# Kernel optimization log

Hardware: AMD Instinct MI355X
Metric: run time of the kernel (lower is better)

The kernel has to match this reference:

```python
import jax, jax.numpy as jnp
import numpy as np

L = 3264          # seq_length
K = 12            # ktc=4 -> K=12
LOCC = 4          # ktc=4 -> Locc=4
BLK = 12          # mmse_block_size
DMIN, DMAX = -10, 10  # delay_search_range
RHO = 0.9         # assumed frequency-correlation coefficient for MMSE C matrix


def setup_inputs() -> dict:
    key = jax.random.key(0)
    k1, k2, k3 = jax.random.split(key, 3)
    ls_real = jax.random.normal(k1, (L,), dtype=jnp.float32)
    ls_imag = jax.random.normal(k2, (L,), dtype=jnp.float32)
    cyclic_shifts = jax.random.randint(k3, (8, 4), 0, K, dtype=jnp.int32)
    return {"ls_real": ls_real, "ls_imag": ls_imag, "cyclic_shifts": cyclic_shifts}


def _estimate(ls, cs_flat):
    P = cs_flat.shape[0]  # total ports across all users
    ideal = ((K - cs_flat) % K) * (L // K)                      # [P] ideal CIR peak positions
    h_time = jnp.fft.ifft(ls)
    hmag = jnp.abs(h_time)                                      # [L]
    idx = jnp.arange(L)
    # circular search window [ideal+DMIN, ideal+DMAX] around each ideal peak
    rel = (idx[None, :] - (ideal[:, None] + DMIN)) % L          # [P, L]
    mask = rel <= (DMAX - DMIN)
    vals = jnp.where(mask, hmag[None, :], -jnp.inf)
    peak = jnp.argmax(vals, axis=1)                             # [P]
    d = peak - ideal
    offset = jnp.where((peak > ideal) & (d > L // 2), d - L,
             jnp.where((ideal - peak) > L // 2, d + L, d))
    m = offset + ideal                                          # [P] phasor shift amounts
    # phasor exp(j 2 pi m n / L); reduce m*n mod L to keep fp32 phase accurate
    n = jnp.arange(L)
    phase = (2.0 * np.pi / L) * ((m[:, None] * n[None, :]) % L).astype(jnp.float32)
    phasor = jnp.exp(1j * phase).astype(jnp.complex64)          # [P, L]
    h_up = ls[None, :] * phasor                                 # [P, L]
    # OCC demux: average every LOCC points
    h_avg = h_up.reshape(P, L // LOCC, LOCC).mean(axis=-1)      # [P, L/LOCC]
    # linear interpolation back to L, centers of groups as sample points
    g = LOCC
    orig = (g - 1) / 2.0 + g * jnp.arange(L // g, dtype=jnp.float32)
    new = jnp.arange(L, dtype=jnp.float32)
    interp1 = jax.vmap(lambda r: jnp.interp(new, orig, r))
    h_interp = (interp1(jnp.real(h_avg)) + 1j * interp1(jnp.imag(h_avg))).astype(jnp.complex64)  # [P, L]
    # residual of multi-port reconstruction
    h_recon = jnp.sum(h_interp / phasor, axis=0)
    residual = ls - h_recon
    # noise power from adjacent-tone differences
    diff = ls[1:] - ls[:-1]
    noise_power = jnp.mean(jnp.abs(diff) ** 2) / 2.0
    # add residual back per port
    h_wr = h_interp + residual[None, :] * phasor                # [P, L]
    # block MMSE: h_mmse = C (C + noise I)^{-1} h_block, C[i,j] = rho^{|i-j|}
    ij = jnp.abs(jnp.arange(BLK)[:, None] - jnp.arange(BLK)[None, :])
    C = (RHO ** ij).astype(jnp.float32)
    A = C + noise_power * jnp.eye(BLK, dtype=jnp.float32)
    F = jnp.linalg.solve(A.T, C.T).T                            # F = C @ inv(A), [BLK, BLK]
    blocks = h_wr.reshape(P, L // BLK, BLK)
    h_mmse = jnp.einsum('pbk,jk->pbj', blocks, F.astype(jnp.complex64)).reshape(P, L)
    # the original nested loop emits the same P inner results for each of P outer (u,p)
    return jnp.tile(h_mmse, (P, 1))                             # [P*P, L]


def reference(ls_real, ls_imag, cyclic_shifts):
    ls = (ls_real + 1j * ls_imag).astype(jnp.complex64)
    cs_flat = cyclic_shifts.reshape(-1)
    return _estimate(ls, cs_flat)
```

## Files before the change

kernel.cpp:

```cpp
#include <hip/hip_runtime.h>
#include <math.h>

#define LL    3264
#define KK    12
#define PP    32
#define NW    21
#define DMIN  (-10)
#define GAVG  (LL/4)
#define NBLK  (LL/12)

#define OUT_REAL  (PP*PP*LL)
#define OUT_CPLX  (PP*PP*LL*2)
#define SCRATCH_F 270520

__global__ void k_window_noise(const float* __restrict__ lsr,
                               const float* __restrict__ lsi,
                               const int* __restrict__ cs,
                               double* __restrict__ mag2,
                               double* __restrict__ noise) {
    __shared__ double sre[256], sim[256];
    const int b = blockIdx.x;
    const int tid = threadIdx.x;
    const float c0 = (float)(2.0 * M_PI / (double)LL);
    if (b < PP * NW) {
        const int p = b / NW, r = b % NW;
        const int ideal = ((KK - cs[p]) % KK) * (LL / KK);
        int t = ideal + DMIN + r;
        t %= LL; if (t < 0) t += LL;
        double are = 0.0, aim = 0.0;
        for (int n = tid; n < LL; n += 256) {
            unsigned mod = (unsigned)(n * t) % LL;
            float ang = c0 * (float)mod;
            float ss, cc;
            sincosf(ang, &ss, &cc);
            float xr = lsr[n], xi = lsi[n];
            are += (double)(xr * cc - xi * ss);
            aim += (double)(xr * ss + xi * cc);
        }
        sre[tid] = are; sim[tid] = aim;
        __syncthreads();
        for (int s = 128; s > 0; s >>= 1) {
            if (tid < s) { sre[tid] += sre[tid + s]; sim[tid] += sim[tid + s]; }
            __syncthreads();
        }
        if (tid == 0) mag2[b] = sre[0] * sre[0] + sim[0] * sim[0];
    } else {
        double acc = 0.0;
        for (int n = tid; n < LL - 1; n += 256) {
            double dr = (double)lsr[n + 1] - (double)lsr[n];
            double di = (double)lsi[n + 1] - (double)lsi[n];
            acc += dr * dr + di * di;
        }
        sre[tid] = acc;
        __syncthreads();
        for (int s = 128; s > 0; s >>= 1) {
            if (tid < s) sre[tid] += sre[tid + s];
            __syncthreads();
        }
        if (tid == 0) *noise = sre[0] / (double)(LL - 1) * 0.5;
    }
}

__global__ void k_peak_F(const int* __restrict__ cs,
                         const double* __restrict__ mag2,
                         const double* __restrict__ noise,
                         int* __restrict__ peak,
                         float* __restrict__ F) {
    __shared__ double A[12][12], Y[12][12];
    const int tid = threadIdx.x;

    if (tid < PP) {
        const int ideal = ((KK - cs[tid]) % KK) * (LL / KK);
        double best = -1.0; int bestl = 0x7fffffff;
        for (int r = 0; r < NW; r++) {
            int l = ideal + DMIN + r;
            l %= LL; if (l < 0) l += LL;
            double v = mag2[tid * NW + r];
            if (v > best || (v == best && l < bestl)) { best = v; bestl = l; }
        }
        peak[tid] = bestl;
    }

    const int row = tid / 12, c = tid % 12;
    if (tid < 144) {
        int d = row - c; if (d < 0) d = -d;
        float cij = (float)pow(0.9, (double)d);
        double npow = (double)((float)(*noise));
        A[row][c] = (double)cij + (row == c ? npow : 0.0);
        Y[row][c] = (double)cij;
    }
    __syncthreads();

    for (int col = 0; col < 12; col++) {
        double dinv = 0.0, pa = 0.0, py = 0.0, f = 0.0;
        if (tid < 144) {
            dinv = 1.0 / A[col][col];
            pa = A[col][c]; py = Y[col][c];
            f  = A[row][col];
        }
        __syncthreads();
        if (tid < 144) {
            if (row == col) { A[row][c] = pa * dinv; Y[row][c] = py * dinv; }
            else            { A[row][c] -= (f * dinv) * pa; Y[row][c] -= (f * dinv) * py; }
        }
        __syncthreads();
    }
    if (tid < 144) F[row * 12 + c] = (float)Y[c][row];
}

template <bool CPLX>
__global__ __launch_bounds__(384) void k_fused(const float* __restrict__ lsr,
                                               const float* __restrict__ lsi,
                                               const int* __restrict__ peak,
                                               const float* __restrict__ F,
                                               float* __restrict__ out) {
    const int b = blockIdx.x;
    const int tid = threadIdx.x;
    __shared__ float hav[32][5][2];
    __shared__ float hin[32][12][2];
    __shared__ float pha[32][12][2];
    __shared__ float con[32][12][2];
    __shared__ float w_s[32][12][2];
    __shared__ float res[12][2];
    __shared__ float Fs[144];
    __shared__ int   pk[32];

    if (tid < 144) Fs[tid] = F[tid];
    if (tid < 32)  pk[tid] = peak[tid];
    __syncthreads();

    const int jb3 = 3 * b - 1;
    const int jbase = jb3 < 0 ? 0 : jb3;
    const float c0 = (float)(2.0 * M_PI / (double)LL);

    if (tid < 160) {
        const int p = tid / 5, js = tid % 5;
        int j = jbase + js; if (j > GAVG - 1) j = GAVG - 1;
        const int m = pk[p];
        float ar = 0.f, ai = 0.f;
        for (int s = 0; s < 4; s++) {
            int n = j * 4 + s;
            unsigned mod = (unsigned)(m * n) % LL;
            float ang = c0 * (float)mod;
            float ss, cc;
            sincosf(ang, &ss, &cc);
            float xr = lsr[n], xi = lsi[n];
            ar += xr * cc - xi * ss;
            ai += xr * ss + xi * cc;
        }
        hav[p][js][0] = ar * 0.25f;
        hav[p][js][1] = ai * 0.25f;
    }
    __syncthreads();

    {
        const int p = tid / 12, k = tid % 12;
        const int x = b * 12 + k;
        float re, im;
        if (x < 2)            { re = hav[p][0][0]; im = hav[p][0][1]; }
        else if (x >= LL - 2) { int js = (GAVG - 1) - jbase;
                                re = hav[p][js][0]; im = hav[p][js][1]; }
        else {
            int j = (x - 2) >> 2, js = j - jbase;
            float t = ((float)x - (1.5f + 4.0f * (float)j)) * 0.25f;
            float r0 = hav[p][js][0],     i0 = hav[p][js][1];
            float r1 = hav[p][js + 1][0], i1 = hav[p][js + 1][1];
            re = r0 + t * (r1 - r0);
            im = i0 + t * (i1 - i0);
        }
        hin[p][k][0] = re; hin[p][k][1] = im;
        const int m = pk[p];
        unsigned mod = (unsigned)(m * x) % LL;
        float ang = c0 * (float)mod;
        float ss, cc;
        sincosf(ang, &ss, &cc);
        pha[p][k][0] = cc; pha[p][k][1] = ss;
        float den = cc * cc + ss * ss;
        con[p][k][0] = (re * cc + im * ss) / den;
        con[p][k][1] = (im * cc - re * ss) / den;
    }
    __syncthreads();

    if (tid < 24) {
        const int k = tid >> 1, c = tid & 1;
        float s = 0.f;
        for (int p = 0; p < 32; p++) s += con[p][k][c];
        const int n = b * 12 + k;
        res[k][c] = (c ? lsi[n] : lsr[n]) - s;
    }
    __syncthreads();

    {
        const int p = tid / 12, k = tid % 12;
        float rr = res[k][0], ri = res[k][1];
        float cc = pha[p][k][0], ss = pha[p][k][1];
        w_s[p][k][0] = hin[p][k][0] + rr * cc - ri * ss;
        w_s[p][k][1] = hin[p][k][1] + rr * ss + ri * cc;
    }
    __syncthreads();

    {
        const int p = tid / 12, j = tid % 12;
        float ar = 0.f, ai = 0.f;
        for (int k = 0; k < 12; k++) {
            float f = Fs[j * 12 + k];
            ar += f * w_s[p][k][0];
            ai += f * w_s[p][k][1];
        }
        if (CPLX) {
            const size_t off = ((size_t)p * LL + (size_t)b * 12 + j) * 2;
            for (int q = 0; q < PP; q++) {
                out[(size_t)q * PP * LL * 2 + off]     = ar;
                out[(size_t)q * PP * LL * 2 + off + 1] = ai;
            }
        } else {
            const size_t off = (size_t)p * LL + (size_t)b * 12 + j;
            for (int q = 0; q < PP; q++)
                out[(size_t)q * PP * LL + off] = ar;
        }
    }
}

__global__ void k_havg(const float* __restrict__ lsr, const float* __restrict__ lsi,
                       const int* __restrict__ peak, float* __restrict__ havg) {
    const int idx = blockIdx.x * blockDim.x + threadIdx.x;
    if (idx >= PP * GAVG) return;
    const int p = idx / GAVG, jj = idx % GAVG;
    const int m = peak[p];
    const float c0 = (float)(2.0 * M_PI / (double)LL);
    float ar = 0.f, ai = 0.f;
    for (int s = 0; s < 4; s++) {
        int n = jj * 4 + s;
        unsigned mod = (unsigned)(m * n) % LL;
        float ph = c0 * (float)mod;
        float ss, cc;
        sincosf(ph, &ss, &cc);
        float xr = lsr[n], xi = lsi[n];
        ar += xr * cc - xi * ss;
        ai += xr * ss + xi * cc;
    }
    havg[idx * 2]     = ar * 0.25f;
    havg[idx * 2 + 1] = ai * 0.25f;
}

__global__ void k_interp(const float* __restrict__ havg, float* __restrict__ hinterp) {
    const int idx = blockIdx.x * blockDim.x + threadIdx.x;
    if (idx >= PP * LL) return;
    const int p = idx / LL, x = idx % LL;
    const float* hp = havg + (size_t)p * GAVG * 2;
    float re, im;
    if (x < 2) { re = hp[0]; im = hp[1]; }
    else if (x >= LL - 2) { re = hp[(GAVG - 1) * 2]; im = hp[(GAVG - 1) * 2 + 1]; }
    else {
        int j = (x - 2) >> 2;
        float t = ((float)x - (1.5f + 4.0f * (float)j)) * 0.25f;
        float r0 = hp[j * 2],       i0 = hp[j * 2 + 1];
        float r1 = hp[(j + 1) * 2], i1 = hp[(j + 1) * 2 + 1];
        re = r0 + t * (r1 - r0);
        im = i0 + t * (i1 - i0);
    }
    hinterp[idx * 2]     = re;
    hinterp[idx * 2 + 1] = im;
}

__global__ void k_resid(const float* __restrict__ lsr, const float* __restrict__ lsi,
                        const int* __restrict__ peak, const float* __restrict__ hinterp,
                        float* __restrict__ resid) {
    const int l = blockIdx.x * blockDim.x + threadIdx.x;
    if (l >= LL) return;
    const float c0 = (float)(2.0 * M_PI / (double)LL);
    float sr = 0.f, si = 0.f;
    for (int p = 0; p < PP; p++) {
        int m = peak[p];
        unsigned mod = (unsigned)(m * l) % LL;
        float ph = c0 * (float)mod;
        float ss, cc;
        sincosf(ph, &ss, &cc);
        float hr = hinterp[((size_t)p * LL + l) * 2];
        float hi = hinterp[((size_t)p * LL + l) * 2 + 1];
        float den = cc * cc + ss * ss;
        sr += (hr * cc + hi * ss) / den;
        si += (hi * cc - hr * ss) / den;
    }
    resid[l * 2]     = lsr[l] - sr;
    resid[l * 2 + 1] = lsi[l] - si;
}

template <bool CPLX>
__global__ void k_mmse(const int* __restrict__ peak, const float* __restrict__ hinterp,
                       const float* __restrict__ resid, const float* __restrict__ F,
                       float* __restrict__ out) {
    const int idx = blockIdx.x * blockDim.x + threadIdx.x;
    if (idx >= PP * NBLK) return;
    const int p = idx / NBLK, b = idx % NBLK;
    const int m = peak[p];
    const float c0 = (float)(2.0 * M_PI / (double)LL);
    float wr[12], wi[12];
    for (int k = 0; k < 12; k++) {
        int n = b * 12 + k;
        unsigned mod = (unsigned)(m * n) % LL;
        float ph = c0 * (float)mod;
        float ss, cc;
        sincosf(ph, &ss, &cc);
        float rr = resid[n * 2], ri = resid[n * 2 + 1];
        wr[k] = hinterp[((size_t)p * LL + n) * 2]     + (rr * cc - ri * ss);
        wi[k] = hinterp[((size_t)p * LL + n) * 2 + 1] + (rr * ss + ri * cc);
    }
    for (int j = 0; j < 12; j++) {
        float ar = 0.f, ai = 0.f;
        for (int k = 0; k < 12; k++) {
            float f = F[j * 12 + k];
            ar += f * wr[k];
            ai += f * wi[k];
        }
        if (CPLX) {
            float* orow = out + (size_t)p * LL * 2 + (size_t)b * 24;
            orow[j * 2]     = ar;
            orow[j * 2 + 1] = ai;
        } else {
            out[(size_t)p * LL + (size_t)b * 12 + j] = ar;
        }
    }
}

__global__ void k_tile(float4* __restrict__ out, int tile_f4) {
    const int idx = blockIdx.x * blockDim.x + threadIdx.x;
    if (idx >= tile_f4) return;
    float4 v = out[idx];
    for (int q = 1; q < PP; q++)
        out[(size_t)q * tile_f4 + idx] = v;
}

extern "C" void kernel_launch(void* const* d_in, const int* in_sizes, int n_in,
                              void* d_out, int out_size, void* d_ws, size_t ws_size,
                              hipStream_t stream) {
    const float* lsr = (const float*)d_in[0];
    const float* lsi = (const float*)d_in[1];
    const int*   cs  = (const int*)d_in[2];
    float* out = (float*)d_out;
    const bool cplx = (out_size >= OUT_CPLX);

    if (ws_size >= 16384) {
        double* mag2  = (double*)d_ws;
        double* noise = mag2 + PP * NW;
        int*    peak  = (int*)(noise + 1);
        float*  F     = (float*)(peak + PP);

        k_window_noise<<<PP * NW + 1, 256, 0, stream>>>(lsr, lsi, cs, mag2, noise);
        k_peak_F<<<1, 192, 0, stream>>>(cs, mag2, noise, peak, F);
        if (cplx) k_fused<true ><<<NBLK, 384, 0, stream>>>(lsr, lsi, peak, F, out);
        else      k_fused<false><<<NBLK, 384, 0, stream>>>(lsr, lsi, peak, F, out);
    } else {
        float* base = out + ((size_t)out_size - SCRATCH_F);
        double* mag2  = (double*)base;
        double* noise = mag2 + PP * NW;
        int*    peak  = (int*)(base + 2692);
        float*  F     = base + 2724;
        float*  havg  = base + 2868;
        float*  hint  = base + 55092;
        float*  resid = base + 263988;

        k_window_noise<<<PP * NW + 1, 256, 0, stream>>>(lsr, lsi, cs, mag2, noise);
        k_peak_F<<<1, 192, 0, stream>>>(cs, mag2, noise, peak, F);
        k_havg<<<(PP * GAVG + 255) / 256, 256, 0, stream>>>(lsr, lsi, peak, havg);
        k_interp<<<(PP * LL + 255) / 256, 256, 0, stream>>>(havg, hint);
        k_resid<<<(LL + 255) / 256, 256, 0, stream>>>(lsr, lsi, peak, hint, resid);
        if (cplx) {
            k_mmse<true><<<(PP * NBLK + 255) / 256, 256, 0, stream>>>(peak, hint, resid, F, out);
            const int tile_f4 = PP * LL * 2 / 4;
            k_tile<<<(tile_f4 + 255) / 256, 256, 0, stream>>>((float4*)out, tile_f4);
        } else {
            k_mmse<false><<<(PP * NBLK + 255) / 256, 256, 0, stream>>>(peak, hint, resid, F, out);
            const int tile_f4 = PP * LL / 4;
            k_tile<<<(tile_f4 + 255) / 256, 256, 0, stream>>>((float4*)out, tile_f4);
        }
    }
}
```

Before: 28.23 us.

## Dedupe window DFTs by ideal, fuse peak/F solve, vectorize tiled output stores

The window DFT magnitudes are now computed once per distinct ideal position (12) rather than per port (32). The separate peak-selection kernel is removed: the noise block now solves for the MMSE filter, and each fused block picks peaks itself. The fused kernel stages its output tile in shared memory and writes the 32 tiled copies with coalesced float4 stores instead of scalar strided writes. This cuts a launch, reduces DFT work, and improves store efficiency, at the cost of redundant peak searches in every block.

Result: faster. 26.50 us (-6.1%).

```diff
diff --git a/kernel.cpp b/kernel.cpp
--- a/kernel.cpp
+++ b/kernel.cpp
@@ -8,16 +8,225 @@
 #define DMIN  (-10)
 #define GAVG  (LL/4)
 #define NBLK  (LL/12)
+#define NIDE  12
+#define NMAG  (NIDE*NW)
 
 #define OUT_REAL  (PP*PP*LL)
 #define OUT_CPLX  (PP*PP*LL*2)
 #define SCRATCH_F 270520
 
-__global__ void k_window_noise(const float* __restrict__ lsr,
-                               const float* __restrict__ lsi,
-                               const int* __restrict__ cs,
-                               double* __restrict__ mag2,
-                               double* __restrict__ noise) {
+__global__ void k_win_noise_F(const float* __restrict__ lsr,
+                              const float* __restrict__ lsi,
+                              double* __restrict__ mag2,
+                              float* __restrict__ F) {
+    __shared__ double sre[256], sim[256];
+    const int b = blockIdx.x;
+    const int tid = threadIdx.x;
+    const float c0 = (float)(2.0 * M_PI / (double)LL);
+    if (b < NMAG) {
+        const int i = b / NW, r = b % NW;
+        int t = i * (LL / KK) + DMIN + r;
+        t %= LL; if (t < 0) t += LL;
+        double are = 0.0, aim = 0.0;
+        for (int n = tid; n < LL; n += 256) {
+            unsigned mod = (unsigned)(n * t) % LL;
+            float ang = c0 * (float)mod;
+            float ss, cc;
+            sincosf(ang, &ss, &cc);
+            float xr = lsr[n], xi = lsi[n];
+            are += (double)(xr * cc - xi * ss);
+            aim += (double)(xr * ss + xi * cc);
+        }
+        sre[tid] = are; sim[tid] = aim;
+        __syncthreads();
+        for (int s = 128; s > 0; s >>= 1) {
+            if (tid < s) { sre[tid] += sre[tid + s]; sim[tid] += sim[tid + s]; }
+            __syncthreads();
+        }
+        if (tid == 0) mag2[b] = sre[0] * sre[0] + sim[0] * sim[0];
+    } else {
+        double acc = 0.0;
+        for (int n = tid; n < LL - 1; n += 256) {
+            double dr = (double)lsr[n + 1] - (double)lsr[n];
+            double di = (double)lsi[n + 1] - (double)lsi[n];
+            acc += dr * dr + di * di;
+        }
+        sre[tid] = acc;
+        __syncthreads();
+        for (int s = 128; s > 0; s >>= 1) {
+            if (tid < s) sre[tid] += sre[tid + s];
+            __syncthreads();
+        }
+        if (tid == 0) sre[0] = (double)((float)(sre[0] / (double)(LL - 1) * 0.5));
+        __syncthreads();
+        const double npow = sre[0];
+
+        __shared__ double A[12][12], Y[12][12];
+        const int row = tid / 12, c = tid % 12;
+        if (tid < 144) {
+            int d = row - c; if (d < 0) d = -d;
+            float cij = (float)pow(0.9, (double)d);
+            A[row][c] = (double)cij + (row == c ? npow : 0.0);
+            Y[row][c] = (double)cij;
+        }
+        __syncthreads();
+        for (int col = 0; col < 12; col++) {
+            double dinv = 0.0, pa = 0.0, py = 0.0, f = 0.0;
+            if (tid < 144) {
+                dinv = 1.0 / A[col][col];
+                pa = A[col][c]; py = Y[col][c];
+                f  = A[row][col];
+            }
+            __syncthreads();
+            if (tid < 144) {
+                if (row == col) { A[row][c] = pa * dinv; Y[row][c] = py * dinv; }
+                else            { A[row][c] -= (f * dinv) * pa; Y[row][c] -= (f * dinv) * py; }
+            }
+            __syncthreads();
+        }
+        if (tid < 144) F[row * 12 + c] = (float)Y[c][row];
+    }
+}
+
+template <bool CPLX>
+__global__ __launch_bounds__(384) void k_fused(const float* __restrict__ lsr,
+                                               const float* __restrict__ lsi,
+                                               const int* __restrict__ cs,
+                                               const double* __restrict__ mag2,
+                                               const float* __restrict__ Fg,
+                                               float* __restrict__ out) {
+    const int b = blockIdx.x;
+    const int tid = threadIdx.x;
+    __shared__ float hav[32][5][2];
+    __shared__ float hin[32][12][2];
+    __shared__ float pha[32][12][2];
+    __shared__ float con[32][12][2];
+    __shared__ float w_s[32][12][2];
+    __shared__ float res[12][2];
+    __shared__ float Fs[144];
+    __shared__ int   pk[32];
+    __shared__ __align__(16) float smo[768];
+
+    if (tid < 144) Fs[tid] = Fg[tid];
+    if (tid < 32) {
+        const int idl = (KK - cs[tid]) % KK;
+        const int ideal = idl * (LL / KK);
+        double best = -1.0; int bestl = 0x7fffffff;
+        for (int r = 0; r < NW; r++) {
+            int l = ideal + DMIN + r;
+            l %= LL; if (l < 0) l += LL;
+            double v = mag2[idl * NW + r];
+            if (v > best || (v == best && l < bestl)) { best = v; bestl = l; }
+        }
+        pk[tid] = bestl;
+    }
+    __syncthreads();
+
+    const int jb3 = 3 * b - 1;
+    const int jbase = jb3 < 0 ? 0 : jb3;
+    const float c0 = (float)(2.0 * M_PI / (double)LL);
+
+    if (tid < 160) {
+        const int p = tid / 5, js = tid % 5;
+        int j = jbase + js; if (j > GAVG - 1) j = GAVG - 1;
+        const int m = pk[p];
+        float ar = 0.f, ai = 0.f;
+        for (int s = 0; s < 4; s++) {
+            int n = j * 4 + s;
+            unsigned mod = (unsigned)(m * n) % LL;
+            float ang = c0 * (float)mod;
+            float ss, cc;
+            sincosf(ang, &ss, &cc);
+            float xr = lsr[n], xi = lsi[n];
+            ar += xr * cc - xi * ss;
+            ai += xr * ss + xi * cc;
+        }
+        hav[p][js][0] = ar * 0.25f;
+        hav[p][js][1] = ai * 0.25f;
+    }
+    __syncthreads();
+
+    {
+        const int p = tid / 12, k = tid % 12;
+        const int x = b * 12 + k;
+        float re, im;
+        if (x < 2)            { re = hav[p][0][0]; im = hav[p][0][1]; }
+        else if (x >= LL - 2) { int js = (GAVG - 1) - jbase;
+                                re = hav[p][js][0]; im = hav[p][js][1]; }
+        else {
+            int j = (x - 2) >> 2, js = j - jbase;
+            float t = ((float)x - (1.5f + 4.0f * (float)j)) * 0.25f;
+            float r0 = hav[p][js][0],     i0 = hav[p][js][1];
+            float r1 = hav[p][js + 1][0], i1 = hav[p][js + 1][1];
+            re = r0 + t * (r1 - r0);
+            im = i0 + t * (i1 - i0);
+        }
+        hin[p][k][0] = re; hin[p][k][1] = im;
+        const int m = pk[p];
+        unsigned mod = (unsigned)(m * x) % LL;
+        float ang = c0 * (float)mod;
+        float ss, cc;
+        sincosf(ang, &ss, &cc);
+        pha[p][k][0] = cc; pha[p][k][1] = ss;
+        float den = cc * cc + ss * ss;
+        con[p][k][0] = (re * cc + im * ss) / den;
+        con[p][k][1] = (im * cc - re * ss) / den;
+    }
+    __syncthreads();
+
+    if (tid < 24) {
+        const int k = tid >> 1, c = tid & 1;
+        float s = 0.f;
+        for (int p = 0; p < 32; p++) s += con[p][k][c];
+        const int n = b * 12 + k;
+        res[k][c] = (c ? lsi[n] : lsr[n]) - s;
+    }
+    __syncthreads();
+
+    {
+        const int p = tid / 12, k = tid % 12;
+        float rr = res[k][0], ri = res[k][1];
+        float cc = pha[p][k][0], ss = pha[p][k][1];
+        w_s[p][k][0] = hin[p][k][0] + rr * cc - ri * ss;
+        w_s[p][k][1] = hin[p][k][1] + rr * ss + ri * cc;
+    }
+    __syncthreads();
+
+    {
+        const int p = tid / 12, j = tid % 12;
+        float ar = 0.f, ai = 0.f;
+        for (int k = 0; k < 12; k++) {
+            float f = Fs[j * 12 + k];
+            ar += f * w_s[p][k][0];
+            ai += f * w_s[p][k][1];
+        }
+        if (CPLX) { smo[(p * 12 + j) * 2] = ar; smo[(p * 12 + j) * 2 + 1] = ai; }
+        else      { smo[p * 12 + j] = ar; }
+    }
+    __syncthreads();
+
+    const float4* smo4 = (const float4*)smo;
+    float4* out4 = (float4*)out;
+    if (CPLX) {
+        for (int idx = tid; idx < 32 * 192; idx += 384) {
+            const int q = idx / 192, c = idx % 192;
+            const int p = c / 6, w = c % 6;
+            out4[(size_t)q * (PP * LL * 2 / 4) + p * (LL / 2) + b * 6 + w] = smo4[c];
+        }
+    } else {
+        for (int idx = tid; idx < 32 * 96; idx += 384) {
+            const int q = idx / 96, c = idx % 96;
+            const int p = c / 3, w = c % 3;
+            out4[(size_t)q * (PP * LL / 4) + p * (LL / 4) + b * 3 + w] = smo4[c];
+        }
+    }
+}
+
+__global__ void k_window_noise_fb(const float* __restrict__ lsr,
+                                  const float* __restrict__ lsi,
+                                  const int* __restrict__ cs,
+                                  double* __restrict__ mag2,
+                                  double* __restrict__ noise) {
     __shared__ double sre[256], sim[256];
     const int b = blockIdx.x;
     const int tid = threadIdx.x;
@@ -61,14 +270,13 @@
     }
 }
 
-__global__ void k_peak_F(const int* __restrict__ cs,
-                         const double* __restrict__ mag2,
-                         const double* __restrict__ noise,
-                         int* __restrict__ peak,
-                         float* __restrict__ F) {
+__global__ void k_peak_F_fb(const int* __restrict__ cs,
+                            const double* __restrict__ mag2,
+                            const double* __restrict__ noise,
+                            int* __restrict__ peak,
+                            float* __restrict__ F) {
     __shared__ double A[12][12], Y[12][12];
     const int tid = threadIdx.x;
-
     if (tid < PP) {
         const int ideal = ((KK - cs[tid]) % KK) * (LL / KK);
         double best = -1.0; int bestl = 0x7fffffff;
@@ -80,7 +288,6 @@
         }
         peak[tid] = bestl;
     }
-
     const int row = tid / 12, c = tid % 12;
     if (tid < 144) {
         int d = row - c; if (d < 0) d = -d;
@@ -90,7 +297,6 @@
         Y[row][c] = (double)cij;
     }
     __syncthreads();
-
     for (int col = 0; col < 12; col++) {
         double dinv = 0.0, pa = 0.0, py = 0.0, f = 0.0;
         if (tid < 144) {
@@ -106,119 +312,6 @@
         __syncthreads();
     }
     if (tid < 144) F[row * 12 + c] = (float)Y[c][row];
-}
-
-template <bool CPLX>
-__global__ __launch_bounds__(384) void k_fused(const float* __restrict__ lsr,
-                                               const float* __restrict__ lsi,
-                                               const int* __restrict__ peak,
-                                               const float* __restrict__ F,
-                                               float* __restrict__ out) {
-    const int b = blockIdx.x;
-    const int tid = threadIdx.x;
-    __shared__ float hav[32][5][2];
-    __shared__ float hin[32][12][2];
-    __shared__ float pha[32][12][2];
-    __shared__ float con[32][12][2];
-    __shared__ float w_s[32][12][2];
-    __shared__ float res[12][2];
-    __shared__ float Fs[144];
-    __shared__ int   pk[32];
-
-    if (tid < 144) Fs[tid] = F[tid];
-    if (tid < 32)  pk[tid] = peak[tid];
-    __syncthreads();
-
-    const int jb3 = 3 * b - 1;
-    const int jbase = jb3 < 0 ? 0 : jb3;
-    const float c0 = (float)(2.0 * M_PI / (double)LL);
-
-    if (tid < 160) {
-        const int p = tid / 5, js = tid % 5;
-        int j = jbase + js; if (j > GAVG - 1) j = GAVG - 1;
-        const int m = pk[p];
-        float ar = 0.f, ai = 0.f;
-        for (int s = 0; s < 4; s++) {
-            int n = j * 4 + s;
-            unsigned mod = (unsigned)(m * n) % LL;
-            float ang = c0 * (float)mod;
-            float ss, cc;
-            sincosf(ang, &ss, &cc);
-            float xr = lsr[n], xi = lsi[n];
-            ar += xr * cc - xi * ss;
-            ai += xr * ss + xi * cc;
-        }
-        hav[p][js][0] = ar * 0.25f;
-        hav[p][js][1] = ai * 0.25f;
-    }
-    __syncthreads();
-
-    {
-        const int p = tid / 12, k = tid % 12;
-        const int x = b * 12 + k;
-        float re, im;
-        if (x < 2)            { re = hav[p][0][0]; im = hav[p][0][1]; }
-        else if (x >= LL - 2) { int js = (GAVG - 1) - jbase;
-                                re = hav[p][js][0]; im = hav[p][js][1]; }
-        else {
-            int j = (x - 2) >> 2, js = j - jbase;
-            float t = ((float)x - (1.5f + 4.0f * (float)j)) * 0.25f;
-            float r0 = hav[p][js][0],     i0 = hav[p][js][1];
-            float r1 = hav[p][js + 1][0], i1 = hav[p][js + 1][1];
-            re = r0 + t * (r1 - r0);
-            im = i0 + t * (i1 - i0);
-        }
-        hin[p][k][0] = re; hin[p][k][1] = im;
-        const int m = pk[p];
-        unsigned mod = (unsigned)(m * x) % LL;
-        float ang = c0 * (float)mod;
-        float ss, cc;
-        sincosf(ang, &ss, &cc);
-        pha[p][k][0] = cc; pha[p][k][1] = ss;
-        float den = cc * cc + ss * ss;
-        con[p][k][0] = (re * cc + im * ss) / den;
-        con[p][k][1] = (im * cc - re * ss) / den;
-    }
-    __syncthreads();
-
-    if (tid < 24) {
-        const int k = tid >> 1, c = tid & 1;
-        float s = 0.f;
-        for (int p = 0; p < 32; p++) s += con[p][k][c];
-        const int n = b * 12 + k;
-        res[k][c] = (c ? lsi[n] : lsr[n]) - s;
-    }
-    __syncthreads();
-
-    {
-        const int p = tid / 12, k = tid % 12;
-        float rr = res[k][0], ri = res[k][1];
-        float cc = pha[p][k][0], ss = pha[p][k][1];
-        w_s[p][k][0] = hin[p][k][0] + rr * cc - ri * ss;
-        w_s[p][k][1] = hin[p][k][1] + rr * ss + ri * cc;
-    }
-    __syncthreads();
-
-    {
-        const int p = tid / 12, j = tid % 12;
-        float ar = 0.f, ai = 0.f;
-        for (int k = 0; k < 12; k++) {
-            float f = Fs[j * 12 + k];
-            ar += f * w_s[p][k][0];
-            ai += f * w_s[p][k][1];
-        }
-        if (CPLX) {
-            const size_t off = ((size_t)p * LL + (size_t)b * 12 + j) * 2;
-            for (int q = 0; q < PP; q++) {
-                out[(size_t)q * PP * LL * 2 + off]     = ar;
-                out[(size_t)q * PP * LL * 2 + off + 1] = ai;
-            }
-        } else {
-            const size_t off = (size_t)p * LL + (size_t)b * 12 + j;
-            for (int q = 0; q < PP; q++)
-                out[(size_t)q * PP * LL + off] = ar;
-        }
-    }
 }
 
 __global__ void k_havg(const float* __restrict__ lsr, const float* __restrict__ lsi,
@@ -341,15 +434,12 @@
     const bool cplx = (out_size >= OUT_CPLX);
 
     if (ws_size >= 16384) {
-        double* mag2  = (double*)d_ws;
-        double* noise = mag2 + PP * NW;
-        int*    peak  = (int*)(noise + 1);
-        float*  F     = (float*)(peak + PP);
-
-        k_window_noise<<<PP * NW + 1, 256, 0, stream>>>(lsr, lsi, cs, mag2, noise);
-        k_peak_F<<<1, 192, 0, stream>>>(cs, mag2, noise, peak, F);
-        if (cplx) k_fused<true ><<<NBLK, 384, 0, stream>>>(lsr, lsi, peak, F, out);
-        else      k_fused<false><<<NBLK, 384, 0, stream>>>(lsr, lsi, peak, F, out);
+        double* mag2 = (double*)d_ws;
+        float*  F    = (float*)(mag2 + NMAG);
+
+        k_win_noise_F<<<NMAG + 1, 256, 0, stream>>>(lsr, lsi, mag2, F);
+        if (cplx) k_fused<true ><<<NBLK, 384, 0, stream>>>(lsr, lsi, cs, mag2, F, out);
+        else      k_fused<false><<<NBLK, 384, 0, stream>>>(lsr, lsi, cs, mag2, F, out);
     } else {
         float* base = out + ((size_t)out_size - SCRATCH_F);
         double* mag2  = (double*)base;
@@ -360,8 +450,8 @@
         float*  hint  = base + 55092;
         float*  resid = base + 263988;
 
-        k_window_noise<<<PP * NW + 1, 256, 0, stream>>>(lsr, lsi, cs, mag2, noise);
-        k_peak_F<<<1, 192, 0, stream>>>(cs, mag2, noise, peak, F);
+        k_window_noise_fb<<<PP * NW + 1, 256, 0, stream>>>(lsr, lsi, cs, mag2, noise);
+        k_peak_F_fb<<<1, 192, 0, stream>>>(cs, mag2, noise, peak, F);
         k_havg<<<(PP * GAVG + 255) / 256, 256, 0, stream>>>(lsr, lsi, peak, havg);
         k_interp<<<(PP * LL + 255) / 256, 256, 0, stream>>>(havg, hint);
         k_resid<<<(LL + 255) / 256, 256, 0, stream>>>(lsr, lsi, peak, hint, resid);
```
